# Optimization experiments

Hardware: AMD Instinct MI355X
Metric: run time of the kernel (lower is better)

The kernel has to match this reference:

```python
import jax, jax.numpy as jnp
import numpy as np
from jax.scipy.special import logsumexp

N_STATES = 512
VOCAB = 10000
BATCH = 64
T_MAX = 1024


def setup_inputs() -> dict:
    key = jax.random.key(0)
    k1, k2, k3, k4, k5 = jax.random.split(key, 5)
    x = jax.random.randint(k1, (BATCH, T_MAX), 0, VOCAB)
    T = jax.random.randint(k2, (BATCH,), 1, T_MAX + 1)  # lengths in [1, T_max]
    priors = jax.random.normal(k3, (N_STATES,), dtype=jnp.float32)
    trans = jax.random.normal(k4, (N_STATES, N_STATES), dtype=jnp.float32)
    emit = jax.random.normal(k5, (N_STATES, VOCAB), dtype=jnp.float32)
    return {"x": x, "T": T, "priors": priors, "trans": trans, "emit": emit}


def reference(x, T, priors, trans, emit):
    # x: (B, Tmax) int, T: (B,) int lengths
    log_pi = jax.nn.log_softmax(priors)            # (N,)
    log_T = jax.nn.log_softmax(trans, axis=0)      # (N, N), columns normalized (dim=0 in torch)
    log_E = jax.nn.log_softmax(emit, axis=1)       # (N, M)

    em = log_E.T[x]                                # (B, Tmax, N) emission log-probs per timestep
    la0 = em[:, 0] + log_pi                        # (B, N)

    def step(la_prev, em_t):
        # out[b, j] = logsumexp_k log_T[j, k] + la_prev[b, k]
        la_new = em_t + logsumexp(log_T[None, :, :] + la_prev[:, None, :], axis=2)
        return la_new, logsumexp(la_new, axis=1)   # carry, per-step log-sum over states

    _, sums = jax.lax.scan(step, la0, jnp.moveaxis(em[:, 1:], 1, 0))  # sums: (Tmax-1, B)
    log_sums = jnp.concatenate([logsumexp(la0, axis=1)[None, :], sums], axis=0)  # (Tmax, B)

    idx = jnp.clip(T, 1, x.shape[1]) - 1           # (B,)
    log_probs = jnp.take_along_axis(log_sums.T, idx[:, None], axis=1)  # (B, 1)
    return log_probs
```

## Files before the change

### kernel.cpp

```cpp
#include <hip/hip_runtime.h>
#include <hip/hip_bf16.h>


typedef unsigned long long u64;
typedef unsigned int u32;
typedef unsigned short u16;
using f32x4 = __attribute__((ext_vector_type(4))) float;
using i32x8 = __attribute__((ext_vector_type(8))) int;

#define N_ST 512
#define VOCAB 10000
#define BATCH 64
#define T_MAX 1024

#define WS_EB       0
#define WS_GB       10240000
#define WS_A8       20480000
#define WS_ROWLSE   20742144
#define WS_COLLSE   20744192
#define WS_PINORM   20746240

static __device__ __forceinline__ float bf16f(u16 h) {
    return __uint_as_float((u32)h << 16);
}
static __device__ __forceinline__ u16 bf16enc(float f) {
    u32 u = __float_as_uint(f);
    return (u16)((u + 0x7fffu + ((u >> 16) & 1u)) >> 16);
}

static __device__ __forceinline__ float dec8(u32 b) {
    float nrm = __uint_as_float((b << 20) + 0x3C000000u);
    float dnm = (float)b * 0x1p-9f;
    return b >= 8u ? nrm : dnm;
}

static __device__ __forceinline__ u32 enc_e4m3(float f) {
    if (!(f > 0.f)) return 0u;
    unsigned u = __float_as_uint(f);
    int e = (int)((u >> 23) & 0xff) - 127;
    unsigned m = u & 0x7fffffu;
    if (e > 8 || (e == 8 && m >= 0x700000u)) return 0x7eu;
    if (e >= -6) {
        unsigned mant = m >> 20;
        unsigned rest = m & 0xfffffu;
        if (rest > 0x80000u || (rest == 0x80000u && (mant & 1u))) mant++;
        unsigned r = ((unsigned)(e + 7) << 3) + mant;
        return r > 0x7eu ? 0x7eu : r;
    }
    if (e < -10) return 0u;
    unsigned full = 0x800000u | m;
    int shift = 23 - (e + 9);
    unsigned r = full >> shift;
    unsigned rem = full & ((1u << shift) - 1u);
    unsigned half = 1u << (shift - 1);
    if (rem > half || (rem == half && (r & 1u))) r++;
    return r;
}

template <bool HI>
static __device__ __forceinline__ u32 cvtpk2(float a, float b, u32 old) {
#if __has_builtin(__builtin_amdgcn_cvt_pk_fp8_f32)
    return (u32)__builtin_amdgcn_cvt_pk_fp8_f32(a, b, (int)old, HI);
#else
    unsigned v = enc_e4m3(a) | (enc_e4m3(b) << 8);
    return HI ? ((old & 0x0000ffffu) | (v << 16)) : ((old & 0xffff0000u) | v);
#endif
}

__global__ __launch_bounds__(256) void k_row_lse(const float* __restrict__ emit,
                                                 float* __restrict__ rowLSE) {
    const int n = blockIdx.x;
    const float* row = emit + (size_t)n * VOCAB;
    __shared__ float redm[4], reds[4];
    const int tid = threadIdx.x, lane = tid & 63, wid = tid >> 6;

    float m = -INFINITY;
    for (int i = tid; i < VOCAB; i += 256) m = fmaxf(m, row[i]);
    #pragma unroll
    for (int o = 32; o; o >>= 1) m = fmaxf(m, __shfl_down(m, o));
    if (lane == 0) redm[wid] = m;
    __syncthreads();
    if (tid == 0) redm[0] = fmaxf(fmaxf(redm[0], redm[1]), fmaxf(redm[2], redm[3]));
    __syncthreads();
    m = redm[0];

    float s = 0.f;
    for (int i = tid; i < VOCAB; i += 256) s += __expf(row[i] - m);
    #pragma unroll
    for (int o = 32; o; o >>= 1) s += __shfl_down(s, o);
    if (lane == 0) reds[wid] = s;
    __syncthreads();
    if (tid == 0) rowLSE[n] = m + __logf(reds[0] + reds[1] + reds[2] + reds[3]);
}

__global__ __launch_bounds__(256) void k_expEmitT(const float* __restrict__ emit,
                                                  const float* __restrict__ rowLSE,
                                                  u16* __restrict__ Eb) {
    __shared__ float tile[64][65];
    const int m0 = blockIdx.x * 64;
    const int n0 = blockIdx.y * 64;
    const int tid = threadIdx.x;

    #pragma unroll
    for (int it = 0; it < 16; ++it) {
        const int idx = it * 256 + tid;
        const int mm = idx & 63, nn = idx >> 6;
        const int m = m0 + mm;
        tile[nn][mm] = (m < VOCAB) ? emit[(size_t)(n0 + nn) * VOCAB + m] : 0.f;
    }
    __syncthreads();
    #pragma unroll
    for (int it = 0; it < 16; ++it) {
        const int idx = it * 256 + tid;
        const int nn = idx & 63, mm = idx >> 6;
        const int m = m0 + mm;
        if (m < VOCAB)
            Eb[(size_t)m * N_ST + n0 + nn] =
                bf16enc(__expf(tile[nn][mm] - rowLSE[n0 + nn]));
    }
}

__global__ __launch_bounds__(256) void k_col_lse(const float* __restrict__ trans,
                                                 float* __restrict__ colLSE) {
    const int k = blockIdx.x;
    const int tid = threadIdx.x, lane = tid & 63, wid = tid >> 6;
    __shared__ float redm[4], reds[4];

    float a = trans[(size_t)tid * N_ST + k];
    float b = trans[(size_t)(tid + 256) * N_ST + k];
    float m = fmaxf(a, b);
    #pragma unroll
    for (int o = 32; o; o >>= 1) m = fmaxf(m, __shfl_down(m, o));
    if (lane == 0) redm[wid] = m;
    __syncthreads();
    if (tid == 0) redm[0] = fmaxf(fmaxf(redm[0], redm[1]), fmaxf(redm[2], redm[3]));
    __syncthreads();
    m = redm[0];

    float s = __expf(a - m) + __expf(b - m);
    #pragma unroll
    for (int o = 32; o; o >>= 1) s += __shfl_down(s, o);
    if (lane == 0) reds[wid] = s;
    __syncthreads();
    if (tid == 0) colLSE[k] = m + __logf(reds[0] + reds[1] + reds[2] + reds[3]);
}

__global__ __launch_bounds__(64) void k_packA_fp8(const float* __restrict__ trans,
                                                  const float* __restrict__ colLSE,
                                                  u32* __restrict__ A8) {
    const int f = blockIdx.x;
    const int l = threadIdx.x;
    const int w = f >> 4, ks = (f >> 2) & 3, jt = f & 3;
    const int j = w * 64 + jt * 16 + (l & 15);
    const int k0 = ks * 128 + (l >> 4) * 32;
    u32 dw[8];
    #pragma unroll
    for (int d = 0; d < 8; ++d) {
        float a0 = 256.0f * __expf(trans[(size_t)j * N_ST + k0 + 4 * d + 0] - colLSE[k0 + 4 * d + 0]);
        float a1 = 256.0f * __expf(trans[(size_t)j * N_ST + k0 + 4 * d + 1] - colLSE[k0 + 4 * d + 1]);
        float a2 = 256.0f * __expf(trans[(size_t)j * N_ST + k0 + 4 * d + 2] - colLSE[k0 + 4 * d + 2]);
        float a3 = 256.0f * __expf(trans[(size_t)j * N_ST + k0 + 4 * d + 3] - colLSE[k0 + 4 * d + 3]);
        u32 pk = cvtpk2<false>(a0, a1, 0u);
        dw[d] = cvtpk2<true>(a2, a3, pk);
    }
    u32* dst = A8 + (size_t)f * 512 + l * 8;
    *(uint4*)dst       = make_uint4(dw[0], dw[1], dw[2], dw[3]);
    *(uint4*)(dst + 4) = make_uint4(dw[4], dw[5], dw[6], dw[7]);
}

__global__ __launch_bounds__(512) void k_pinorm(const float* __restrict__ priors,
                                                float* __restrict__ pinorm) {
    const int j = threadIdx.x, lane = j & 63, wid = j >> 6;
    __shared__ float redm[8], reds[8];
    float v = priors[j];

    float m = v;
    #pragma unroll
    for (int o = 32; o; o >>= 1) m = fmaxf(m, __shfl_down(m, o));
    if (lane == 0) redm[wid] = m;
    __syncthreads();
    if (j == 0) {
        float r = redm[0];
        for (int i = 1; i < 8; ++i) r = fmaxf(r, redm[i]);
        redm[0] = r;
    }
    __syncthreads();
    m = redm[0];

    float s = __expf(v - m);
    #pragma unroll
    for (int o = 32; o; o >>= 1) s += __shfl_down(s, o);
    if (lane == 0) reds[wid] = s;
    __syncthreads();
    if (j == 0) {
        float r = 0.f;
        for (int i = 0; i < 8; ++i) r += reds[i];
        reds[0] = r;
    }
    __syncthreads();
    pinorm[j] = __expf(v - m) / reds[0];
}

__global__ __launch_bounds__(256) void k_G(const u16* __restrict__ Eb,
                                           const float* __restrict__ trans,
                                           const float* __restrict__ colLSE,
                                           u16* __restrict__ Gb) {
    __shared__ float Es[16][512];
    const int m0 = blockIdx.x * 16;
    const int tid = threadIdx.x;
    for (int idx = tid; idx < 16 * 512; idx += 256)
        Es[idx >> 9][idx & 511] = bf16f(Eb[(size_t)(m0 + (idx >> 9)) * 512 + (idx & 511)]);
    __syncthreads();

    const int k0 = tid, k1 = tid + 256;
    const float c0 = colLSE[k0], c1 = colLSE[k1];
    float acc0[16], acc1[16];
    #pragma unroll
    for (int mi = 0; mi < 16; ++mi) { acc0[mi] = 0.f; acc1[mi] = 0.f; }

    for (int j4 = 0; j4 < 128; ++j4) {
        float a0[4], a1[4];
        #pragma unroll
        for (int d = 0; d < 4; ++d) {
            a0[d] = __expf(trans[(size_t)(4 * j4 + d) * N_ST + k0] - c0);
            a1[d] = __expf(trans[(size_t)(4 * j4 + d) * N_ST + k1] - c1);
        }
        #pragma unroll
        for (int mi = 0; mi < 16; ++mi) {
            const f32x4 e = *(const f32x4*)&Es[mi][4 * j4];
            acc0[mi] = fmaf(e[0], a0[0], fmaf(e[1], a0[1],
                       fmaf(e[2], a0[2], fmaf(e[3], a0[3], acc0[mi]))));
            acc1[mi] = fmaf(e[0], a1[0], fmaf(e[1], a1[1],
                       fmaf(e[2], a1[2], fmaf(e[3], a1[3], acc1[mi]))));
        }
    }
    #pragma unroll
    for (int mi = 0; mi < 16; ++mi) {
        Gb[(size_t)(m0 + mi) * N_ST + k0] = bf16enc(acc0[mi]);
        Gb[(size_t)(m0 + mi) * N_ST + k1] = bf16enc(acc1[mi]);
    }
}

#define UNIT_SCALES 0x7f7f7f7f
#define LN256 5.545177444479562f

#define WG_BARRIER()                                        \
  {                                                         \
    asm volatile("s_waitcnt lgkmcnt(0)" ::: "memory");      \
    __builtin_amdgcn_s_barrier();                           \
    asm volatile("" ::: "memory");                          \
  }

#define STEP_BODY(EU, GU, EP, GP)                                               \
  {                                                                             \
    const int xpre = xnext;                                                     \
    GP = *(const uint4*)((const char*)Gb + ((size_t)xpre << 10) + (l << 4));    \
    _Pragma("unroll")                                                           \
    for (int jt = 0; jt < 4; ++jt)                                              \
      EP[jt] = *(const u64*)(Eb + (size_t)xpre * N_ST + wbase + jt * 16 + rbase); \
    xnext = xb[(t + 2 <= Tf) ? (t + 2) : Tf];                                   \
    const u64 vown = vq[p][l];                                                  \
    const u32* vbase = (const u32*)&vq[p][0];                                   \
    i32x8 bq[4];                                                                \
    _Pragma("unroll")                                                           \
    for (int ks = 0; ks < 4; ++ks) {                                            \
      const uint4 b0 = *(const uint4*)(vbase + ks * 32 + grp * 8);              \
      const uint4 b1 = *(const uint4*)(vbase + ks * 32 + grp * 8 + 4);          \
      bq[ks] = i32x8{(int)b0.x, (int)b0.y, (int)b0.z, (int)b0.w,                \
                     (int)b1.x, (int)b1.y, (int)b1.z, (int)b1.w};               \
    }                                                                           \
    f32x4 aA0={0,0,0,0}, aA1={0,0,0,0}, aA2={0,0,0,0}, aA3={0,0,0,0};           \
    f32x4 aB0={0,0,0,0}, aB1={0,0,0,0}, aB2={0,0,0,0}, aB3={0,0,0,0};           \
    _Pragma("unroll")                                                           \
    for (int kk = 0; kk < 2; ++kk) {                                            \
      const int ksA = kk * 2, ksB = kk * 2 + 1;                                 \
      aA0 = __builtin_amdgcn_mfma_scale_f32_16x16x128_f8f6f4(                   \
                af[ksA * 4 + 0], bq[ksA], aA0, 0, 0, 0, UNIT_SCALES, 0, UNIT_SCALES); \
      aB0 = __builtin_amdgcn_mfma_scale_f32_16x16x128_f8f6f4(                   \
                af[ksB * 4 + 0], bq[ksB], aB0, 0, 0, 0, UNIT_SCALES, 0, UNIT_SCALES); \
      aA1 = __builtin_amdgcn_mfma_scale_f32_16x16x128_f8f6f4(                   \
                af[ksA * 4 + 1], bq[ksA], aA1, 0, 0, 0, UNIT_SCALES, 0, UNIT_SCALES); \
      aB1 = __builtin_amdgcn_mfma_scale_f32_16x16x128_f8f6f4(                   \
                af[ksB * 4 + 1], bq[ksB], aB1, 0, 0, 0, UNIT_SCALES, 0, UNIT_SCALES); \
      aA2 = __builtin_amdgcn_mfma_scale_f32_16x16x128_f8f6f4(                   \
                af[ksA * 4 + 2], bq[ksA], aA2, 0, 0, 0, UNIT_SCALES, 0, UNIT_SCALES); \
      aB2 = __builtin_amdgcn_mfma_scale_f32_16x16x128_f8f6f4(                   \
                af[ksB * 4 + 2], bq[ksB], aB2, 0, 0, 0, UNIT_SCALES, 0, UNIT_SCALES); \
      aA3 = __builtin_amdgcn_mfma_scale_f32_16x16x128_f8f6f4(                   \
                af[ksA * 4 + 3], bq[ksA], aA3, 0, 0, 0, UNIT_SCALES, 0, UNIT_SCALES); \
      aB3 = __builtin_amdgcn_mfma_scale_f32_16x16x128_f8f6f4(                   \
                af[ksB * 4 + 3], bq[ksB], aB3, 0, 0, 0, UNIT_SCALES, 0, UNIT_SCALES); \
    }                                                                           \
    float gv = 0.f;                                                             \
    {                                                                           \
      const u32 gw[4] = {GU.x, GU.y, GU.z, GU.w};                               \
      _Pragma("unroll")                                                         \
      for (int i = 0; i < 4; ++i) {                                             \
        float g0 = bf16f((u16)(gw[i] & 0xffffu));                               \
        float g1 = bf16f((u16)(gw[i] >> 16));                                   \
        float v0 = dec8((u32)(vown >> (16 * i)) & 0xffu);                       \
        float v1 = dec8((u32)(vown >> (16 * i + 8)) & 0xffu);                   \
        gv = fmaf(g0, v0, gv);                                                  \
        gv = fmaf(g1, v1, gv);                                                  \
      }                                                                         \
      _Pragma("unroll")                                                         \
      for (int o = 1; o <= 32; o <<= 1) gv += __shfl_xor(gv, o);                \
    }                                                                           \
    float wv2[16];                                                              \
    _Pragma("unroll")                                                           \
    for (int r = 0; r < 4; ++r) {                                               \
      wv2[0 + r]  = bf16f((u16)(EU[0] >> (16 * r))) * (aA0[r] + aB0[r]);        \
      wv2[4 + r]  = bf16f((u16)(EU[1] >> (16 * r))) * (aA1[r] + aB1[r]);        \
      wv2[8 + r]  = bf16f((u16)(EU[2] >> (16 * r))) * (aA2[r] + aB2[r]);        \
      wv2[12 + r] = bf16f((u16)(EU[3] >> (16 * r))) * (aA3[r] + aB3[r]);        \
    }                                                                           \
    if (t == Tf) {                                                              \
      float s2 = 0.f;                                                           \
      _Pragma("unroll")                                                         \
      for (int i = 0; i < 16; ++i) s2 += wv2[i];                                \
      s2 += __shfl_xor(s2, 16);                                                 \
      s2 += __shfl_xor(s2, 32);                                                 \
      if (l == 0) red[wid] = s2;                                                \
      __syncthreads();                                                          \
      const float Se = red[0] + red[1] + red[2] + red[3] +                      \
                       red[4] + red[5] + red[6] + red[7];                       \
      if (tid == 0) out[b] = L + __logf(Se) - (float)Tb * LN256;                \
    } else {                                                                    \
      L += __logf(gv);                                                          \
      const float sc = 1.0f / gv;                                               \
      if ((l & 15) == 0) {                                                      \
        u32* vw = (u32*)&vq[p ^ 1][0];                                          \
        _Pragma("unroll")                                                       \
        for (int jt = 0; jt < 4; ++jt) {                                        \
          u32 pk = cvtpk2<false>(wv2[jt * 4 + 0] * sc, wv2[jt * 4 + 1] * sc, 0u); \
          pk = cvtpk2<true>(wv2[jt * 4 + 2] * sc, wv2[jt * 4 + 3] * sc, pk);    \
          vw[(wbase >> 2) + jt * 4 + grp] = pk;                                 \
        }                                                                       \
      }                                                                         \
      WG_BARRIER();                                                             \
      p ^= 1;                                                                   \
    }                                                                           \
  }

__global__ __launch_bounds__(512, 2) void hmm_main(const int* __restrict__ x,
                                                   const int* __restrict__ T,
                                                   const u16* __restrict__ Eb,
                                                   const u32* __restrict__ A8,
                                                   const u16* __restrict__ Gb,
                                                   const float* __restrict__ pinorm,
                                                   float* __restrict__ out) {
    __shared__ u64 vq[2][64];
    __shared__ float red[8];
    const int b = blockIdx.x;
    const int tid = threadIdx.x;
    const int l = tid & 63;
    const int wid = tid >> 6;
    const int grp = l >> 4;
    const int wbase = wid * 64;
    const int rbase = grp * 4;

    int Tb = T[b];
    Tb = Tb < 1 ? 1 : (Tb > T_MAX ? T_MAX : Tb);
    const int* xb = x + (size_t)b * T_MAX;

    i32x8 af[16];
    {
        const u32* ap = A8 + (size_t)wid * 16 * 512 + l * 8;
        #pragma unroll
        for (int i = 0; i < 16; ++i) {
            uint4 lo = *(const uint4*)(ap + (size_t)i * 512);
            uint4 hi = *(const uint4*)(ap + (size_t)i * 512 + 4);
            af[i] = i32x8{(int)lo.x, (int)lo.y, (int)lo.z, (int)lo.w,
                          (int)hi.x, (int)hi.y, (int)hi.z, (int)hi.w};
        }
    }

    const int x0 = xb[0];
    const int x1 = xb[1];
    u64 eA[4], eB[4];
    uint4 gA, gB;
    gA = *(const uint4*)((const char*)Gb + ((size_t)x1 << 10) + (l << 4));
    #pragma unroll
    for (int jt = 0; jt < 4; ++jt)
        eA[jt] = *(const u64*)(Eb + (size_t)x1 * N_ST + wbase + jt * 16 + rbase);

    float wv[16];
    float s = 0.f;
    #pragma unroll
    for (int jt = 0; jt < 4; ++jt) {
        u64 eraw = *(const u64*)(Eb + (size_t)x0 * N_ST + wbase + jt * 16 + rbase);
        #pragma unroll
        for (int r = 0; r < 4; ++r) {
            const int j = wbase + jt * 16 + rbase + r;
            float e = bf16f((u16)(eraw >> (16 * r)));
            float t0 = e * pinorm[j];
            wv[jt * 4 + r] = t0;
            s += t0;
        }
    }
    s += __shfl_xor(s, 16);
    s += __shfl_xor(s, 32);
    if (l == 0) red[wid] = s;
    __syncthreads();
    float S0 = red[0] + red[1] + red[2] + red[3] + red[4] + red[5] + red[6] + red[7];
    float L = __logf(S0);
    if (Tb == 1) {
        if (tid == 0) out[b] = L;
        return;
    }
    __syncthreads();
    {
        const float sc = 256.0f / S0;
        if ((l & 15) == 0) {
            u32* vw = (u32*)&vq[0][0];
            #pragma unroll
            for (int jt = 0; jt < 4; ++jt) {
                u32 pk = cvtpk2<false>(wv[jt * 4 + 0] * sc, wv[jt * 4 + 1] * sc, 0u);
                pk = cvtpk2<true>(wv[jt * 4 + 2] * sc, wv[jt * 4 + 3] * sc, pk);
                vw[(wbase >> 2) + jt * 4 + grp] = pk;
            }
        }
    }
    __syncthreads();

    const int Tf = Tb - 1;
    int p = 0;
    int xnext = xb[(2 <= Tf) ? 2 : Tf];
    for (int t = 1;;) {
        STEP_BODY(eA, gA, eB, gB)
        if (t == Tf) break;
        ++t;
        STEP_BODY(eB, gB, eA, gA)
        if (t == Tf) break;
        ++t;
    }
}

extern "C" void kernel_launch(void* const* d_in, const int* in_sizes, int n_in,
                              void* d_out, int out_size, void* d_ws, size_t ws_size,
                              hipStream_t stream) {
    const int*   x      = (const int*)d_in[0];
    const int*   T      = (const int*)d_in[1];
    const float* priors = (const float*)d_in[2];
    const float* trans  = (const float*)d_in[3];
    const float* emit   = (const float*)d_in[4];
    float* out = (float*)d_out;

    char* ws = (char*)d_ws;
    u16*   Eb     = (u16*)(ws + WS_EB);
    u16*   Gb     = (u16*)(ws + WS_GB);
    u32*   A8     = (u32*)(ws + WS_A8);
    float* rowLSE = (float*)(ws + WS_ROWLSE);
    float* colLSE = (float*)(ws + WS_COLLSE);
    float* pinorm = (float*)(ws + WS_PINORM);

    k_row_lse<<<N_ST, 256, 0, stream>>>(emit, rowLSE);
    {
        dim3 g((VOCAB + 63) / 64, N_ST / 64);
        k_expEmitT<<<g, 256, 0, stream>>>(emit, rowLSE, Eb);
    }
    k_col_lse<<<N_ST, 256, 0, stream>>>(trans, colLSE);
    k_packA_fp8<<<128, 64, 0, stream>>>(trans, colLSE, A8);
    k_pinorm<<<1, 512, 0, stream>>>(priors, pinorm);
    k_G<<<VOCAB / 16, 256, 0, stream>>>(Eb, trans, colLSE, Gb);

    hmm_main<<<BATCH, 512, 0, stream>>>(x, T, Eb, A8, Gb, pinorm, out);
}
```

Before: 1.279 ms.

## Compute emission-transition product G with bf16 MFMA using prepacked transition fragments

Replaces the scalar FMA k_G kernel with an MFMA 16x16x32 bf16 kernel. A new pack kernel precomputes exp(trans - colLSE) in bf16 once, laid out in MFMA B-fragment order, so the exp is no longer recomputed for every output tile. This cuts the ALU cost of the precompute GEMM. In exchange the transition factor is rounded to bf16 before accumulation, and the scattered 2-byte output stores may be inefficient.

```diff
diff --git a/kernel.cpp b/kernel.cpp
--- a/kernel.cpp
+++ b/kernel.cpp
@@ -7,6 +7,7 @@
 typedef unsigned short u16;
 using f32x4 = __attribute__((ext_vector_type(4))) float;
 using i32x8 = __attribute__((ext_vector_type(8))) int;
+using short8 = __attribute__((ext_vector_type(8))) short;
 
 #define N_ST 512
 #define VOCAB 10000
@@ -16,9 +17,10 @@
 #define WS_EB       0
 #define WS_GB       10240000
 #define WS_A8       20480000
-#define WS_ROWLSE   20742144
-#define WS_COLLSE   20744192
-#define WS_PINORM   20746240
+#define WS_ABP      20742144
+#define WS_ROWLSE   21266432
+#define WS_COLLSE   21268480
+#define WS_PINORM   21270528
 
 static __device__ __forceinline__ float bf16f(u16 h) {
     return __uint_as_float((u32)h << 16);
@@ -201,43 +203,46 @@
     pinorm[j] = __expf(v - m) / reds[0];
 }
 
-__global__ __launch_bounds__(256) void k_G(const u16* __restrict__ Eb,
-                                           const float* __restrict__ trans,
-                                           const float* __restrict__ colLSE,
-                                           u16* __restrict__ Gb) {
-    __shared__ float Es[16][512];
-    const int m0 = blockIdx.x * 16;
-    const int tid = threadIdx.x;
-    for (int idx = tid; idx < 16 * 512; idx += 256)
-        Es[idx >> 9][idx & 511] = bf16f(Eb[(size_t)(m0 + (idx >> 9)) * 512 + (idx & 511)]);
-    __syncthreads();
-
-    const int k0 = tid, k1 = tid + 256;
-    const float c0 = colLSE[k0], c1 = colLSE[k1];
-    float acc0[16], acc1[16];
-    #pragma unroll
-    for (int mi = 0; mi < 16; ++mi) { acc0[mi] = 0.f; acc1[mi] = 0.f; }
-
-    for (int j4 = 0; j4 < 128; ++j4) {
-        float a0[4], a1[4];
+__global__ __launch_bounds__(64) void k_packAb(const float* __restrict__ trans,
+                                               const float* __restrict__ colLSE,
+                                               u16* __restrict__ Abp) {
+    const int f = blockIdx.x;
+    const int l = threadIdx.x;
+    const int nt = f >> 4, js = f & 15;
+    const int k = nt * 16 + (l & 15);
+    const int j0 = js * 32 + (l >> 4) * 8;
+    const float c = colLSE[k];
+    short8 v;
+    #pragma unroll
+    for (int i = 0; i < 8; ++i)
+        v[i] = (short)bf16enc(__expf(trans[(size_t)(j0 + i) * N_ST + k] - c));
+    *(short8*)(Abp + (size_t)f * 512 + l * 8) = v;
+}
+
+__global__ __launch_bounds__(64) void k_G_mfma(const u16* __restrict__ Eb,
+                                               const u16* __restrict__ Abp,
+                                               u16* __restrict__ Gb) {
+    const int mt = blockIdx.x;
+    const int l = threadIdx.x;
+    const int m0 = mt * 16;
+    const int row = (l >> 4) * 4;
+    const int col = l & 15;
+
+    short8 ef[16];
+    #pragma unroll
+    for (int js = 0; js < 16; ++js)
+        ef[js] = *(const short8*)(Eb + (size_t)(m0 + (l & 15)) * N_ST + js * 32 + (l >> 4) * 8);
+
+    for (int nt = 0; nt < 32; ++nt) {
+        f32x4 acc = {0.f, 0.f, 0.f, 0.f};
         #pragma unroll
-        for (int d = 0; d < 4; ++d) {
-            a0[d] = __expf(trans[(size_t)(4 * j4 + d) * N_ST + k0] - c0);
-            a1[d] = __expf(trans[(size_t)(4 * j4 + d) * N_ST + k1] - c1);
+        for (int js = 0; js < 16; ++js) {
+            const short8 bf = *(const short8*)(Abp + (size_t)(nt * 16 + js) * 512 + l * 8);
+            acc = __builtin_amdgcn_mfma_f32_16x16x32_bf16(ef[js], bf, acc, 0, 0, 0);
         }
         #pragma unroll
-        for (int mi = 0; mi < 16; ++mi) {
-            const f32x4 e = *(const f32x4*)&Es[mi][4 * j4];
-            acc0[mi] = fmaf(e[0], a0[0], fmaf(e[1], a0[1],
-                       fmaf(e[2], a0[2], fmaf(e[3], a0[3], acc0[mi]))));
-            acc1[mi] = fmaf(e[0], a1[0], fmaf(e[1], a1[1],
-                       fmaf(e[2], a1[2], fmaf(e[3], a1[3], acc1[mi]))));
-        }
-    }
-    #pragma unroll
-    for (int mi = 0; mi < 16; ++mi) {
-        Gb[(size_t)(m0 + mi) * N_ST + k0] = bf16enc(acc0[mi]);
-        Gb[(size_t)(m0 + mi) * N_ST + k1] = bf16enc(acc1[mi]);
+        for (int r = 0; r < 4; ++r)
+            Gb[(size_t)(m0 + row + r) * N_ST + nt * 16 + col] = bf16enc(acc[r]);
     }
 }
 
@@ -450,6 +455,7 @@
     u16*   Eb     = (u16*)(ws + WS_EB);
     u16*   Gb     = (u16*)(ws + WS_GB);
     u32*   A8     = (u32*)(ws + WS_A8);
+    u16*   Abp    = (u16*)(ws + WS_ABP);
     float* rowLSE = (float*)(ws + WS_ROWLSE);
     float* colLSE = (float*)(ws + WS_COLLSE);
     float* pinorm = (float*)(ws + WS_PINORM);
@@ -462,7 +468,8 @@
     k_col_lse<<<N_ST, 256, 0, stream>>>(trans, colLSE);
     k_packA_fp8<<<128, 64, 0, stream>>>(trans, colLSE, A8);
     k_pinorm<<<1, 512, 0, stream>>>(priors, pinorm);
-    k_G<<<VOCAB / 16, 256, 0, stream>>>(Eb, trans, colLSE, Gb);
+    k_packAb<<<512, 64, 0, stream>>>(trans, colLSE, Abp);
+    k_G_mfma<<<VOCAB / 16, 64, 0, stream>>>(Eb, Abp, Gb);
 
     hmm_main<<<BATCH, 512, 0, stream>>>(x, T, Eb, A8, Gb, pinorm, out);
 }
```

New measurement: 1.228 ms. 1.04x faster.
